# Kernel optimization log

Hardware: AMD Instinct MI355X
Metric: run time of the kernel (lower is better)

The kernel has to match this reference:

```python
import jax, jax.numpy as jnp
import numpy as np

N_ROI = 1024
N_CLASS = 21      # num_classes + 1
APP_DIM = 1024
D_F = 128
N_REL = 16
DIM_K = 64
DIM_G = 64


def loc2bbox(src, loc):
    # src, loc: [M,4] with (y0,x0,y1,x1) / (dy,dx,dh,dw)
    h = src[:, 2] - src[:, 0]
    w = src[:, 3] - src[:, 1]
    cy = src[:, 0] + 0.5 * h
    cx = src[:, 1] + 0.5 * w
    ncy = loc[:, 0] * h + cy
    ncx = loc[:, 1] * w + cx
    nh = jnp.exp(loc[:, 2]) * h
    nw = jnp.exp(loc[:, 3]) * w
    return jnp.stack([ncy - 0.5 * nh, ncx - 0.5 * nw,
                      ncy + 0.5 * nh, ncx + 0.5 * nw], axis=1)


def rank_embedding(n, feat_dim, wave_len=1000.0):
    rank = jnp.arange(n, dtype=jnp.float32)[:, None]
    fr = jnp.arange(feat_dim // 2, dtype=jnp.float32)
    dim_mat = 1.0 / (wave_len ** (fr / (feat_dim / 2.0)))
    mul = rank * dim_mat[None, :]
    return jnp.concatenate([jnp.sin(mul), jnp.cos(mul)], axis=-1)  # [n, feat_dim]


def positional_embedding(f_g, dim_g, wave_len=1000.0):
    # f_g: [N,4]; replicates the repo's PositionalEmbedding exactly
    x_min, y_min, x_max, y_max = jnp.split(f_g, 4, axis=1)  # [N,1] each
    cx = (x_min + x_max) * 0.5
    cy = (y_min + y_max) * 0.5
    w = (x_max - x_min) + 1.0
    h = (y_max - y_min) + 1.0
    dx = jnp.log(jnp.maximum(jnp.abs((cx - cx.T) / w), 1e-3))
    dy = jnp.log(jnp.maximum(jnp.abs((cy - cy.T) / h), 1e-3))
    dw = jnp.log(w / w.T)
    dh = jnp.log(h / h.T)
    pos = jnp.stack([dx, dy, dw, dh], axis=-1)               # [N,N,4]
    fr = jnp.arange(dim_g // 8, dtype=jnp.float32)
    dim_mat = 1.0 / (wave_len ** (fr / (dim_g / 8.0)))       # [dim_g/8]
    mul = (100.0 * pos)[..., None] * dim_mat                 # [N,N,4,dim_g/8]
    mul = mul.reshape(pos.shape[0], pos.shape[1], -1)
    return jnp.concatenate([jnp.sin(mul), jnp.cos(mul)], axis=-1)  # [N,N,dim_g]


def setup_inputs():
    key = jax.random.key(0)
    ks = jax.random.split(key, 16)
    yx = jax.random.uniform(ks[0], (N_ROI, 2), minval=0.0, maxval=500.0)
    hw = jax.random.uniform(ks[1], (N_ROI, 2), minval=16.0, maxval=128.0)
    sample_roi = jnp.concatenate([yx, yx + hw], axis=1)      # valid (y0,x0,y1,x1)
    roi_cls_loc = jax.random.normal(ks[2], (N_ROI, N_CLASS * 4)) * 0.5
    roi_score = jax.random.normal(ks[3], (N_ROI, N_CLASS))
    # force no background argmax -> nonzero() filter keeps all N (static shapes)
    roi_score = roi_score.at[:, 0].add(-10.0)
    appearance_features = jax.random.normal(ks[4], (N_ROI, APP_DIM))
    size = jnp.array([600, 800], dtype=jnp.int32)
    s = 0.02
    rank_w = jax.random.normal(ks[5], (APP_DIM, D_F)) * s
    rank_b = jnp.zeros((D_F,), jnp.float32)
    feat_w = jax.random.normal(ks[6], (APP_DIM, D_F)) * s
    feat_b = jnp.zeros((D_F,), jnp.float32)
    logit_w = jax.random.normal(ks[7], (APP_DIM, 1)) * s
    logit_b = jnp.zeros((1,), jnp.float32)
    wg_w = jax.random.normal(ks[8], (N_REL, DIM_G)) * s
    wg_b = jnp.full((N_REL,), 0.1, jnp.float32)  # keep some geo weights > 0
    wk_w = jax.random.normal(ks[9], (N_REL, D_F, DIM_K)) * s
    wk_b = jnp.zeros((N_REL, DIM_K), jnp.float32)
    wq_w = jax.random.normal(ks[10], (N_REL, D_F, DIM_K)) * s
    wq_b = jnp.zeros((N_REL, DIM_K), jnp.float32)
    wv_w = jax.random.normal(ks[11], (N_REL, D_F, DIM_K)) * s
    wv_b = jnp.zeros((N_REL, DIM_K), jnp.float32)
    return {"sample_roi": sample_roi, "roi_cls_loc": roi_cls_loc,
            "roi_score": roi_score, "appearance_features": appearance_features,
            "size": size,
            "rank_w": rank_w, "rank_b": rank_b, "feat_w": feat_w, "feat_b": feat_b,
            "logit_w": logit_w, "logit_b": logit_b,
            "wg_w": wg_w, "wg_b": wg_b, "wk_w": wk_w, "wk_b": wk_b,
            "wq_w": wq_w, "wq_b": wq_b, "wv_w": wv_w, "wv_b": wv_b}


def reference(sample_roi, roi_cls_loc, roi_score, appearance_features, size,
              rank_w, rank_b, feat_w, feat_b, logit_w, logit_b,
              wg_w, wg_b, wk_w, wk_b, wq_w, wq_b, wv_w, wv_b):
    n = sample_roi.shape[0]
    size_f = size.astype(jnp.float32)
    # loc denormalization (mean = 0)
    std = jnp.tile(jnp.array([0.1, 0.1, 0.2, 0.2], jnp.float32), N_CLASS)
    loc = (roi_cls_loc * std).reshape(-1, 4)                  # [N*21,4]
    roi_rep = jnp.broadcast_to(sample_roi[:, None, :], (n, N_CLASS, 4)).reshape(-1, 4)
    cls_bbox = loc2bbox(roi_rep, loc).reshape(n, N_CLASS, 4)
    # replicates original's clamp on class-strided slices of the [N,21,4] view
    cls_bbox = cls_bbox.at[:, 0::2].set(jnp.clip(cls_bbox[:, 0::2], 0.0, size_f[0]))
    cls_bbox = cls_bbox.at[:, 1::2].set(jnp.clip(cls_bbox[:, 1::2], 0.0, size_f[1]))
    prob_all = jax.nn.softmax(roi_score, axis=1)
    prob = jnp.max(prob_all, axis=-1)
    prob_argmax = jnp.argmax(prob_all, axis=-1)
    cls_bbox = cls_bbox[jnp.arange(n), prob_argmax]           # [N,4]
    # background filter; inputs guarantee all foreground -> static size n
    nz = jnp.nonzero(prob_argmax, size=n, fill_value=0)[0]
    prob_argmax = prob_argmax[nz]
    prob = prob[nz]
    cls_bbox = cls_bbox[nz]
    feats = appearance_features[nz]
    order = jnp.argsort(-prob)                                # descending
    sorted_prob = prob[order]
    sorted_cls_bboxes = cls_bbox[order]
    sorted_labels = prob_argmax[order]
    sorted_features = feats[order]
    nms_rank = rank_embedding(n, APP_DIM) @ rank_w + rank_b   # [N,D_F]
    emb_feat = sorted_features @ feat_w + feat_b + nms_rank   # [N,D_F]
    pos_emb = positional_embedding(sorted_cls_bboxes, DIM_G)  # [N,N,DIM_G]
    # 16 independent RelationUnits, batched as heads h
    w_g = jax.nn.relu(jnp.einsum('mng,hg->hmn', pos_emb, wg_w) + wg_b[:, None, None])
    k = jnp.einsum('nd,hdk->hnk', emb_feat, wk_w) + wk_b[:, None, :]
    q = jnp.einsum('nd,hdk->hnk', emb_feat, wq_w) + wq_b[:, None, :]
    v = jnp.einsum('nd,hdk->hnk', emb_feat, wv_w) + wv_b[:, None, :]
    # scaled_dot[m,n] = k_m . q_n (row m is 'key', softmax over n) per original
    scores = jnp.einsum('hmk,hnk->hmn', k, q) / np.sqrt(DIM_K).astype(np.float32)
    w_mn = jax.nn.softmax(jnp.log(jnp.maximum(w_g, 1e-6)) + scores, axis=-1)
    rel = jnp.einsum('hmn,hnk->hmk', w_mn, v)                 # [H,N,K]
    rel = rel.transpose(1, 0, 2).reshape(n, N_REL * DIM_K) + sorted_features
    s1 = jax.nn.sigmoid(rel @ logit_w + logit_b).reshape(-1)
    nms_scores = s1 * sorted_prob
    return nms_scores, sorted_labels - 1, sorted_cls_bboxes
```

## Files before the change

kernel.cpp:

```cpp
#include <hip/hip_runtime.h>
#include <hip/hip_bf16.h>
#include <math.h>

typedef unsigned long long u64;
typedef unsigned int u32;
typedef __hip_bfloat16 bf16;

#define N 1024
#define NCLS 21
#define APP 1024
#define DF 128
#define NH 16
#define DK 64
#define NS 4

typedef __attribute__((ext_vector_type(8))) short short8v;
typedef __attribute__((ext_vector_type(4))) float float4v;
union U4S8 { uint4 u; short8v s; };

__device__ __forceinline__ float b2f(bf16 x) { return __bfloat162float(x); }
__device__ __forceinline__ ushort f2bu(float x) { bf16 b = __float2bfloat16(x); return *(ushort*)&b; }
__device__ __forceinline__ float bu2f(ushort u) { return __uint_as_float(((uint)u) << 16); }

__global__ void k_prep(const float* __restrict__ roi, const float* __restrict__ cls_loc,
                       const float* __restrict__ score, const int* __restrict__ size,
                       const float* __restrict__ wgw,
                       float* __restrict__ prob, int* __restrict__ label,
                       float* __restrict__ bbox, u64* __restrict__ keys,
                       ushort* __restrict__ wgwb)
{
    int i = blockIdx.x * 256 + threadIdx.x;
    if (i >= N) return;
    wgwb[i] = f2bu(wgw[i]);

    float s[NCLS];
    float mx = -1e30f; int am = 0;
    for (int c = 0; c < NCLS; c++) {
        s[c] = score[i * NCLS + c];
        if (s[c] > mx) { mx = s[c]; am = c; }
    }
    float sum = 0.f;
    for (int c = 0; c < NCLS; c++) sum += expf(s[c] - mx);
    float p = 1.0f / sum;

    float y0 = roi[i*4+0], x0 = roi[i*4+1];
    float y1 = roi[i*4+2], x1 = roi[i*4+3];
    float hh = y1 - y0, ww = x1 - x0;
    float cy = y0 + 0.5f * hh, cx = x0 + 0.5f * ww;
    float l0 = cls_loc[i*84 + am*4 + 0] * 0.1f;
    float l1 = cls_loc[i*84 + am*4 + 1] * 0.1f;
    float l2 = cls_loc[i*84 + am*4 + 2] * 0.2f;
    float l3 = cls_loc[i*84 + am*4 + 3] * 0.2f;
    float ncy = l0 * hh + cy, ncx = l1 * ww + cx;
    float nh = expf(l2) * hh, nw = expf(l3) * ww;
    float b0 = ncy - 0.5f * nh, b1 = ncx - 0.5f * nw;
    float b2v = ncy + 0.5f * nh, b3 = ncx + 0.5f * nw;
    float lim = ((am & 1) == 0) ? (float)size[0] : (float)size[1];
    b0  = fminf(fmaxf(b0, 0.f), lim);
    b1  = fminf(fmaxf(b1, 0.f), lim);
    b2v = fminf(fmaxf(b2v, 0.f), lim);
    b3  = fminf(fmaxf(b3, 0.f), lim);
    prob[i] = p; label[i] = am;
    bbox[i*4+0] = b0; bbox[i*4+1] = b1; bbox[i*4+2] = b2v; bbox[i*4+3] = b3;
    keys[i] = ((u64)(0xFFFFFFFFu - __float_as_uint(p)) << 32) | (u32)i;
}

__global__ void __launch_bounds__(256) k_rank(
        const u64* __restrict__ keys, const float* __restrict__ prob,
        const int* __restrict__ label, const float* __restrict__ bbox,
        int* __restrict__ order, float* __restrict__ sprob,
        float* __restrict__ sbbox, float* __restrict__ sgeo,
        float* __restrict__ out)
{
    __shared__ u64 sk[N];
    int t = threadIdx.x;
    int i = blockIdx.x * 256 + t;
    for (int j = t; j < N; j += 256) sk[j] = keys[j];
    __syncthreads();
    u64 my = sk[i];
    int r = 0;
    for (int j = 0; j < N; j++) r += (sk[j] < my) ? 1 : 0;
    order[r] = i;
    sprob[r] = prob[i];
    float b0 = bbox[i*4+0], b1 = bbox[i*4+1], b2 = bbox[i*4+2], b3 = bbox[i*4+3];
    sbbox[r*4+0] = b0; sbbox[r*4+1] = b1; sbbox[r*4+2] = b2; sbbox[r*4+3] = b3;
    sgeo[r*4+0] = (b0 + b2) * 0.5f;
    sgeo[r*4+1] = (b1 + b3) * 0.5f;
    sgeo[r*4+2] = __logf(b2 - b0 + 1.0f);
    sgeo[r*4+3] = __logf(b3 - b1 + 1.0f);
    out[N + r] = (float)(label[i] - 1);
    out[2*N + r*4 + 0] = b0;
    out[2*N + r*4 + 1] = b1;
    out[2*N + r*4 + 2] = b2;
    out[2*N + r*4 + 3] = b3;
}

__global__ void __launch_bounds__(256) k_geoemb(
        const int* __restrict__ order, const float* __restrict__ app,
        const float* __restrict__ feat_w, const float* __restrict__ rank_w,
        float* __restrict__ part,
        const float* __restrict__ sbbox, const float* __restrict__ sgeo,
        const ushort* __restrict__ wgwb,
        const float* __restrict__ wgb, bf16* __restrict__ lw)
{
    __shared__ __align__(16) char smem[27904];
    int bx = blockIdx.x, t = threadIdx.x;
    int w = t >> 6, l = t & 63, l15 = l & 15, quad = l >> 4;

    if (bx >= 256) {
        uint (*sOut)[260] = (uint(*)[260])smem;
        int m = bx - 256;

        float4 mg = *(const float4*)&sgeo[m*4];
        float4 mb = *(const float4*)&sbbox[m*4];
        float wm = mb.z - mb.x + 1.0f, hm = mb.w - mb.y + 1.0f;

        float sC  = (quad == 0) ? mg.x : (quad == 1) ? mg.y : 0.0f;
        float sM  = ((quad & 1) == 0) ? 1e-3f * wm : 1e-3f * hm;
        float sL  = ((quad & 1) == 0) ? mg.z : mg.w;
        float sSg = (quad < 2) ? 100.0f : -100.0f;

        U4S8 Bg0, Bg1;
        const uint4* wg4 = (const uint4*)wgwb;
        Bg0.u = wg4[l15*8 + quad];
        Bg1.u = wg4[l15*8 + 4 + quad];
        float bias = wgb[l15];

        const float dmt[8] = { 1.0f, 0.42169650342f, 0.177827941f, 0.0749894209f,
                               0.0316227766f, 0.01333521432f, 0.00562341325f, 0.00237137371f };

        uint* lwu = (uint*)lw;
        for (int half = 0; half < 2; half++) {
            #pragma unroll 4
            for (int mt2i = 0; mt2i < 8; mt2i++) {
                int mt2 = half*8 + mt2i;
                int n = mt2*64 + w*16 + l15;
                float valn = sgeo[n*4 + quad];
                float lg = __logf(fmaxf(fabsf(sC - valn), sM));
                float lv = (quad < 2) ? lg : valn;
                float P  = sSg * (lv - sL);

                U4S8 Af0, Af1;
                #pragma unroll
                for (int j = 0; j < 4; j++) {
                    float s0, c0, s1, c1;
                    __sincosf(P * dmt[2*j],     &s0, &c0);
                    __sincosf(P * dmt[2*j + 1], &s1, &c1);
                    ((uint*)&Af0)[j] = (uint)f2bu(s0) | ((uint)f2bu(s1) << 16);
                    ((uint*)&Af1)[j] = (uint)f2bu(c0) | ((uint)f2bu(c1) << 16);
                }

                float4v c = (float4v){0.f, 0.f, 0.f, 0.f};
                c = __builtin_amdgcn_mfma_f32_16x16x32_bf16(Af0.s, Bg0.s, c, 0, 0, 0);
                c = __builtin_amdgcn_mfma_f32_16x16x32_bf16(Af1.s, Bg1.s, c, 0, 0, 0);
                float v0 = __logf(fmaxf(c[0] + bias, 1e-6f));
                float v1 = __logf(fmaxf(c[1] + bias, 1e-6f));
                float v2 = __logf(fmaxf(c[2] + bias, 1e-6f));
                float v3 = __logf(fmaxf(c[3] + bias, 1e-6f));
                int pb = mt2i*32 + w*8 + quad*2;
                sOut[l15][pb]     = (uint)f2bu(v0) | ((uint)f2bu(v1) << 16);
                sOut[l15][pb + 1] = (uint)f2bu(v2) | ((uint)f2bu(v3) << 16);
            }
            __syncthreads();
            #pragma unroll
            for (int it = 0; it < 4; it++) {
                int idx = t + it * 256;
                int hh = idx >> 6, col4 = idx & 63;
                uint4 val = *(const uint4*)&sOut[hh][col4*4];
                *(uint4*)&lwu[((size_t)hh << 19) + ((size_t)m << 9) + half*256 + col4*4] = val;
            }
            __syncthreads();
        }
    } else {
        ushort (*sA)[72] = (ushort(*)[72])smem;
        ushort (*sW)[72] = (ushort(*)[72])(smem + 9216);
        int* sOrd = (int*)(smem + 27648);
        int idx0 = bx;
        int rt = idx0 & 15, dg = (idx0 >> 4) & 7, ph = idx0 >> 7;
        int r0 = rt * 64;
        if (t < 64) sOrd[t] = order[r0 + t];
        __syncthreads();

        const float* Wsrc = ph ? rank_w : feat_w;
        float4v acc[8];
        #pragma unroll
        for (int nb = 0; nb < 8; nb++) acc[nb] = (float4v){0.f, 0.f, 0.f, 0.f};

        for (int dc = dg * 2; dc < dg * 2 + 2; dc++) {
            int d0 = dc * 64;
            #pragma unroll
            for (int it = 0; it < 32; it++) {
                int idx = t + it * 256;
                int d = idx >> 7, c = idx & 127;
                sW[c][d] = f2bu(Wsrc[(size_t)(d0 + d) * 128 + c]);
            }
            if (ph == 0) {
                #pragma unroll
                for (int it = 0; it < 16; it++) {
                    int idx = t + it * 256;
                    int r = idx >> 6, d = idx & 63;
                    sA[r][d] = f2bu(app[(size_t)sOrd[r] * 1024 + d0 + d]);
                }
            } else {
                #pragma unroll
                for (int it = 0; it < 16; it++) {
                    int idx = t + it * 256;
                    int r = idx >> 6, d = idx & 63;
                    int dgl = d0 + d;
                    float irow = (float)(r0 + r);
                    float val;
                    if (dgl < 512) val = __sinf(irow * exp2f(-(float)dgl * 0.019464422f));
                    else           val = __cosf(irow * exp2f(-(float)(dgl - 512) * 0.019464422f));
                    sA[r][d] = f2bu(val);
                }
            }
            __syncthreads();
            U4S8 Af0, Af1;
            Af0.u = *(uint4*)&sA[w*16 + l15][quad*8];
            Af1.u = *(uint4*)&sA[w*16 + l15][32 + quad*8];
            #pragma unroll
            for (int nb = 0; nb < 8; nb++) {
                U4S8 Bf0, Bf1;
                Bf0.u = *(uint4*)&sW[nb*16 + l15][quad*8];
                Bf1.u = *(uint4*)&sW[nb*16 + l15][32 + quad*8];
                acc[nb] = __builtin_amdgcn_mfma_f32_16x16x32_bf16(Af0.s, Bf0.s, acc[nb], 0, 0, 0);
                acc[nb] = __builtin_amdgcn_mfma_f32_16x16x32_bf16(Af1.s, Bf1.s, acc[nb], 0, 0, 0);
            }
            __syncthreads();
        }
        #pragma unroll
        for (int reg = 0; reg < 4; reg++) {
            int row = r0 + w*16 + quad*4 + reg;
            #pragma unroll
            for (int nb = 0; nb < 8; nb++)
                part[(((size_t)ph * 8 + dg) * 1024 + row) * 128 + nb*16 + l15] = acc[nb][reg];
        }
    }
}

__global__ void k_embsum(const float* __restrict__ part,
                         const float* __restrict__ feat_b, const float* __restrict__ rank_b,
                         bf16* __restrict__ embb)
{
    int gid = blockIdx.x * 256 + threadIdx.x;
    int c = gid & 127;
    float acc = feat_b[c] + rank_b[c];
    #pragma unroll
    for (int p8 = 0; p8 < 16; p8++) acc += part[(size_t)p8 * 131072 + gid];
    embb[gid] = __float2bfloat16(acc);
}

__global__ void __launch_bounds__(256) k_qkv2(
        const bf16* __restrict__ embb,
        const float* __restrict__ wq, const float* __restrict__ bq,
        const float* __restrict__ wk, const float* __restrict__ bk,
        const float* __restrict__ wv, const float* __restrict__ bv,
        bf16* __restrict__ q, bf16* __restrict__ k, bf16* __restrict__ v)
{
    __shared__ ushort sWt[64][136];
    int t = threadIdx.x;
    int rt = blockIdx.x, h = blockIdx.y, mat = blockIdx.z;
    const float* W  = (mat == 0) ? wq : (mat == 1) ? wk : wv;
    const float* Bb = (mat == 0) ? bq : (mat == 1) ? bk : bv;
    bf16* Out       = (mat == 0) ? q  : (mat == 1) ? k  : v;

    #pragma unroll
    for (int i = 0; i < 32; i++) {
        int idx = t + i * 256;
        int d = idx >> 6, kk = idx & 63;
        sWt[kk][d] = f2bu(W[((size_t)h * 128 + d) * 64 + kk]);
    }
    int w = t >> 6, l = t & 63, l15 = l & 15, quad = l >> 4;
    float biasv[4];
    #pragma unroll
    for (int nb = 0; nb < 4; nb++) biasv[nb] = Bb[h * 64 + nb*16 + l15];
    __syncthreads();

    U4S8 Bf[4][4];
    #pragma unroll
    for (int nb = 0; nb < 4; nb++)
        #pragma unroll
        for (int kc = 0; kc < 4; kc++)
            Bf[nb][kc].u = *(uint4*)&sWt[nb*16 + l15][kc*32 + quad*8];

    const uint4* A4 = (const uint4*)embb;
    int r0 = rt * 128 + w * 32;
    ushort* outu = (ushort*)Out;
    for (int mb = 0; mb < 2; mb++) {
        int arow = r0 + mb*16 + l15;
        U4S8 Af[4];
        #pragma unroll
        for (int kc = 0; kc < 4; kc++) Af[kc].u = A4[(size_t)arow * 16 + kc*4 + quad];
        float4v acc[4];
        #pragma unroll
        for (int nb = 0; nb < 4; nb++) acc[nb] = (float4v){0.f, 0.f, 0.f, 0.f};
        #pragma unroll
        for (int kc = 0; kc < 4; kc++)
            #pragma unroll
            for (int nb = 0; nb < 4; nb++)
                acc[nb] = __builtin_amdgcn_mfma_f32_16x16x32_bf16(Af[kc].s, Bf[nb][kc].s, acc[nb], 0, 0, 0);
        #pragma unroll
        for (int reg = 0; reg < 4; reg++) {
            int orow = r0 + mb*16 + quad*4 + reg;
            #pragma unroll
            for (int nb = 0; nb < 4; nb++)
                outu[((size_t)h * N + orow) * 64 + nb*16 + l15] = f2bu(acc[nb][reg] + biasv[nb]);
        }
    }
}

__global__ void __launch_bounds__(256) k_attn4(
        const bf16* __restrict__ q, const bf16* __restrict__ kmat,
        const bf16* __restrict__ v, const bf16* __restrict__ lw,
        bf16* __restrict__ opartb, float* __restrict__ mpart, float* __restrict__ zpart)
{
    __shared__ uint sQu[64][36];
    __shared__ uint sVtu[64][36];
    __shared__ uint slwu[64][36];
    __shared__ uint sPu[4][16][36];

    int t = threadIdx.x;
    int mt = blockIdx.x, h = blockIdx.y, ns = blockIdx.z;
    int m0 = mt * 64;
    int w = t >> 6, l = t & 63, l15 = l & 15, quad = l >> 4;

    U4S8 kf0, kf1;
    {
        const uint4* k4 = (const uint4*)kmat;
        size_t krow = ((size_t)h * N + m0 + w*16 + l15) * 8;
        kf0.u = k4[krow + quad];
        kf1.u = k4[krow + 4 + quad];
    }

    float4v O[4];
    float M[4], Z[4];
    #pragma unroll
    for (int i = 0; i < 4; i++) {
        O[i] = (float4v){0.f, 0.f, 0.f, 0.f};
        M[i] = -1e30f; Z[i] = 0.f;
    }

    const uint* qsrc = (const uint*)q;
    const uint* vsrc = (const uint*)v;
    const uint* lwsrc = (const uint*)lw;

    for (int tile = ns * (16/NS); tile < (ns + 1) * (16/NS); tile++) {
        int n0 = tile * 64;
        #pragma unroll
        for (int i = 0; i < 8; i++) {
            int idx = t + i * 256;
            int nj = idx >> 5, kp = idx & 31;
            sQu[nj][kp] = qsrc[((size_t)h * N + n0 + nj) * 32 + kp];
        }
        #pragma unroll
        for (int i = 0; i < 4; i++) {
            int idx = t + i * 256;
            int a = idx & 31, nh2 = idx >> 5;
            uint g0 = vsrc[((size_t)h * N + n0 + 2*nh2) * 32 + a];
            uint g1 = vsrc[((size_t)h * N + n0 + 2*nh2 + 1) * 32 + a];
            sVtu[2*a][nh2]     = (g0 & 0xFFFFu) | (g1 << 16);
            sVtu[2*a + 1][nh2] = (g0 >> 16) | (g1 & 0xFFFF0000u);
        }
        #pragma unroll
        for (int i = 0; i < 8; i++) {
            int idx = t + i * 256;
            int mi = idx >> 5, np = idx & 31;
            slwu[mi][np] = lwsrc[((size_t)h << 19) + ((size_t)(m0 + mi) << 9) + (n0 >> 1) + np];
        }
        __syncthreads();

        float4v S[4];
        #pragma unroll
        for (int nb = 0; nb < 4; nb++) {
            U4S8 bq0, bq1;
            bq0.u = *(uint4*)&sQu[nb*16 + l15][quad*4];
            bq1.u = *(uint4*)&sQu[nb*16 + l15][16 + quad*4];
            float4v zz = (float4v){0.f, 0.f, 0.f, 0.f};
            float4v p0 = __builtin_amdgcn_mfma_f32_16x16x32_bf16(kf0.s, bq0.s, zz, 0, 0, 0);
            S[nb] = __builtin_amdgcn_mfma_f32_16x16x32_bf16(kf1.s, bq1.s, p0, 0, 0, 0);
        }
        ushort* pRow[4];
        #pragma unroll
        for (int r = 0; r < 4; r++) pRow[r] = (ushort*)&sPu[w][quad*4 + r][0];
        #pragma unroll
        for (int r = 0; r < 4; r++) {
            int mi = w*16 + quad*4 + r;
            float sv[4];
            #pragma unroll
            for (int nb = 0; nb < 4; nb++) {
                int col = nb*16 + l15;
                uint lu = slwu[mi][col >> 1];
                float lv = (col & 1) ? __uint_as_float(lu & 0xFFFF0000u)
                                     : __uint_as_float(lu << 16);
                sv[nb] = S[nb][r] * 0.125f + lv;
            }
            float rm = fmaxf(fmaxf(sv[0], sv[1]), fmaxf(sv[2], sv[3]));
            #pragma unroll
            for (int off = 1; off < 16; off <<= 1)
                rm = fmaxf(rm, __shfl_xor(rm, off, 64));
            float newM = fmaxf(M[r], rm);
            float pr[4], rs = 0.f;
            #pragma unroll
            for (int nb = 0; nb < 4; nb++) {
                pr[nb] = __expf(sv[nb] - newM);
                rs += pr[nb];
            }
            #pragma unroll
            for (int off = 1; off < 16; off <<= 1)
                rs += __shfl_xor(rs, off, 64);
            float sc = __expf(M[r] - newM);
            M[r] = newM;
            Z[r] = Z[r] * sc + rs;
            #pragma unroll
            for (int kvb = 0; kvb < 4; kvb++) O[kvb][r] *= sc;
            #pragma unroll
            for (int nb = 0; nb < 4; nb++)
                pRow[r][nb*16 + l15] = f2bu(pr[nb]);
        }
        {
            U4S8 ap0, ap1;
            ap0.u = *(uint4*)&sPu[w][l15][quad*4];
            ap1.u = *(uint4*)&sPu[w][l15][16 + quad*4];
            #pragma unroll
            for (int kvb = 0; kvb < 4; kvb++) {
                U4S8 bv0, bv1;
                bv0.u = *(uint4*)&sVtu[kvb*16 + l15][quad*4];
                bv1.u = *(uint4*)&sVtu[kvb*16 + l15][16 + quad*4];
                O[kvb] = __builtin_amdgcn_mfma_f32_16x16x32_bf16(ap0.s, bv0.s, O[kvb], 0, 0, 0);
                O[kvb] = __builtin_amdgcn_mfma_f32_16x16x32_bf16(ap1.s, bv1.s, O[kvb], 0, 0, 0);
            }
        }
        __syncthreads();
    }

    ushort* ob = (ushort*)opartb;
    #pragma unroll
    for (int r = 0; r < 4; r++) {
        int m = m0 + w*16 + quad*4 + r;
        size_t row = ((size_t)ns * NH + h) * N + m;
        #pragma unroll
        for (int kvb = 0; kvb < 4; kvb++)
            ob[row * 64 + kvb*16 + l15] = f2bu(O[kvb][r]);
        if (l15 == 0) { mpart[row] = M[r]; zpart[row] = Z[r]; }
    }
}

__global__ void __launch_bounds__(128) k_final2(
        const bf16* __restrict__ opartb, const float* __restrict__ mpart,
        const float* __restrict__ zpart, const int* __restrict__ order,
        const float* __restrict__ app, const float* __restrict__ lw,
        const float* __restrict__ lb, const float* __restrict__ sprob,
        float* __restrict__ out)
{
    __shared__ float sWgt[NH][NS];
    __shared__ float sInvZ[NH];
    __shared__ float red[2];
    int m = blockIdx.x, t = threadIdx.x;
    if (t < NH) {
        int h = t;
        float Ms[NS], Mg = -1e30f;
        #pragma unroll
        for (int ns = 0; ns < NS; ns++) {
            Ms[ns] = mpart[(size_t)ns * 16384 + h * 1024 + m];
            Mg = fmaxf(Mg, Ms[ns]);
        }
        float Zt = 0.f;
        #pragma unroll
        for (int ns = 0; ns < NS; ns++) {
            float wgt = __expf(Ms[ns] - Mg);
            sWgt[h][ns] = wgt;
            Zt += zpart[(size_t)ns * 16384 + h * 1024 + m] * wgt;
        }
        sInvZ[h] = 1.0f / Zt;
    }
    __syncthreads();
    int o = order[m];
    const ushort* ob = (const ushort*)opartb;
    float s = 0.f;
    for (int j = t; j < APP; j += 128) {
        int hh = j >> 6, kk = j & 63;
        size_t base = ((size_t)hh * 1024 + m) * 64 + kk;
        float val = 0.f;
        #pragma unroll
        for (int ns = 0; ns < NS; ns++)
            val += bu2f(ob[(size_t)ns * 1048576 + base]) * sWgt[hh][ns];
        float rv = val * sInvZ[hh] + app[o * APP + j];
        s += rv * lw[j];
    }
    #pragma unroll
    for (int off = 32; off > 0; off >>= 1) s += __shfl_down(s, off, 64);
    if ((t & 63) == 0) red[t >> 6] = s;
    __syncthreads();
    if (t == 0) {
        float tot = red[0] + red[1] + lb[0];
        float s1 = 1.0f / (1.0f + expf(-tot));
        out[m] = s1 * sprob[m];
    }
}

extern "C" void kernel_launch(void* const* d_in, const int* in_sizes, int n_in,
                              void* d_out, int out_size, void* d_ws, size_t ws_size,
                              hipStream_t stream)
{
    const float* roi      = (const float*)d_in[0];
    const float* cls_loc  = (const float*)d_in[1];
    const float* score    = (const float*)d_in[2];
    const float* app      = (const float*)d_in[3];
    const int*   size     = (const int*)d_in[4];
    const float* rank_w   = (const float*)d_in[5];
    const float* rank_b   = (const float*)d_in[6];
    const float* feat_w   = (const float*)d_in[7];
    const float* feat_b   = (const float*)d_in[8];
    const float* logit_w  = (const float*)d_in[9];
    const float* logit_b  = (const float*)d_in[10];
    const float* wg_w     = (const float*)d_in[11];
    const float* wg_b     = (const float*)d_in[12];
    const float* wk_w     = (const float*)d_in[13];
    const float* wk_b     = (const float*)d_in[14];
    const float* wq_w     = (const float*)d_in[15];
    const float* wq_b     = (const float*)d_in[16];
    const float* wv_w     = (const float*)d_in[17];
    const float* wv_b     = (const float*)d_in[18];
    float* out = (float*)d_out;

    char* ws = (char*)d_ws;
    float* prob  = (float*)(ws + 0);
    int*   label = (int*)  (ws + 4096);
    float* bbox  = (float*)(ws + 8192);
    u64*   keys  = (u64*)  (ws + 24576);
    int*   order = (int*)  (ws + 32768);
    float* sprob = (float*)(ws + 36864);
    float* sbbox = (float*)(ws + 40960);
    bf16*  embb  = (bf16*) (ws + 57344);
    ushort* wgwb = (ushort*)(ws + 1048576);
    float* sgeo  = (float*)(ws + 1052672);
    bf16*  q     = (bf16*) (ws + 8970240);
    bf16*  k     = (bf16*) (ws + 11067392);
    bf16*  v     = (bf16*) (ws + 13164544);
    bf16*  lwbuf = (bf16*) (ws + 17358848);
    float* part  = (float*)(ws + 50913280);
    bf16*  opartb= (bf16*) (ws + 67690496);
    float* mpart = (float*)(ws + 84467712);
    float* zpart = (float*)(ws + 84729856);

    k_prep<<<4, 256, 0, stream>>>(roi, cls_loc, score, size, wg_w, prob, label, bbox, keys, wgwb);
    k_rank<<<4, 256, 0, stream>>>(keys, prob, label, bbox, order, sprob, sbbox, sgeo, out);
    k_geoemb<<<1280, 256, 0, stream>>>(order, app, feat_w, rank_w, part,
                                       sbbox, sgeo, wgwb, wg_b, lwbuf);
    k_embsum<<<512, 256, 0, stream>>>(part, feat_b, rank_b, embb);
    k_qkv2<<<dim3(8, 16, 3), 256, 0, stream>>>(embb, wq_w, wq_b, wk_w, wk_b, wv_w, wv_b, q, k, v);
    k_attn4<<<dim3(16, 16, NS), 256, 0, stream>>>(q, k, v, lwbuf, opartb, mpart, zpart);
    k_final2<<<1024, 128, 0, stream>>>(opartb, mpart, zpart, order, app, logit_w, logit_b, sprob, out);
}
```

Baseline: 177.2 us.

## Pre-transpose QKV weights to bf16 once and read Q fragments directly from global

The embedding-sum kernel gets extra blocks that convert and transpose the Q/K/V weights into a bf16 [mat][h][k][d] buffer in workspace. The QKV projection kernel then loads its MFMA B fragments straight from that buffer, with no per-block fp32 transposition through shared memory and no barrier. Separately, the attention kernel stops staging Q tiles in shared memory and loads the Q fragments for each tile directly from global memory. This trades LDS traffic and a sync for more uncoalesced 16-byte global loads, which rely on cache hits.

```diff
diff --git a/kernel.cpp b/kernel.cpp
--- a/kernel.cpp
+++ b/kernel.cpp
@@ -240,48 +240,54 @@
 
 __global__ void k_embsum(const float* __restrict__ part,
                          const float* __restrict__ feat_b, const float* __restrict__ rank_b,
-                         bf16* __restrict__ embb)
-{
-    int gid = blockIdx.x * 256 + threadIdx.x;
-    int c = gid & 127;
-    float acc = feat_b[c] + rank_b[c];
-    #pragma unroll
-    for (int p8 = 0; p8 < 16; p8++) acc += part[(size_t)p8 * 131072 + gid];
-    embb[gid] = __float2bfloat16(acc);
+                         bf16* __restrict__ embb,
+                         const float* __restrict__ wq, const float* __restrict__ wk,
+                         const float* __restrict__ wv, ushort* __restrict__ wqkvt)
+{
+    int b = blockIdx.x, t = threadIdx.x;
+    if (b < 512) {
+        int gid = b * 256 + t;
+        int c = gid & 127;
+        float acc = feat_b[c] + rank_b[c];
+        #pragma unroll
+        for (int p8 = 0; p8 < 16; p8++) acc += part[(size_t)p8 * 131072 + gid];
+        embb[gid] = __float2bfloat16(acc);
+    } else {
+        int lin = (b - 512) * 256 + t;
+        int mat = lin >> 17;
+        int rem = lin & 131071;
+        int h   = rem >> 13;
+        int rem2 = rem & 8191;
+        int kk  = rem2 >> 7;
+        int d   = rem2 & 127;
+        const float* W = (mat == 0) ? wq : (mat == 1) ? wk : wv;
+        wqkvt[lin] = f2bu(W[(((size_t)h * 128 + d) << 6) + kk]);
+    }
 }
 
 __global__ void __launch_bounds__(256) k_qkv2(
-        const bf16* __restrict__ embb,
-        const float* __restrict__ wq, const float* __restrict__ bq,
-        const float* __restrict__ wk, const float* __restrict__ bk,
-        const float* __restrict__ wv, const float* __restrict__ bv,
+        const bf16* __restrict__ embb, const ushort* __restrict__ wqkvt,
+        const float* __restrict__ bq, const float* __restrict__ bk,
+        const float* __restrict__ bv,
         bf16* __restrict__ q, bf16* __restrict__ k, bf16* __restrict__ v)
 {
-    __shared__ ushort sWt[64][136];
     int t = threadIdx.x;
     int rt = blockIdx.x, h = blockIdx.y, mat = blockIdx.z;
-    const float* W  = (mat == 0) ? wq : (mat == 1) ? wk : wv;
     const float* Bb = (mat == 0) ? bq : (mat == 1) ? bk : bv;
     bf16* Out       = (mat == 0) ? q  : (mat == 1) ? k  : v;
-
+    int w = t >> 6, l = t & 63, l15 = l & 15, quad = l >> 4;
+
+    const uint4* Wt4 = (const uint4*)(wqkvt + ((size_t)(mat * 16 + h) << 13));
+    U4S8 Bf[4][4];
     #pragma unroll
-    for (int i = 0; i < 32; i++) {
-        int idx = t + i * 256;
-        int d = idx >> 6, kk = idx & 63;
-        sWt[kk][d] = f2bu(W[((size_t)h * 128 + d) * 64 + kk]);
-    }
-    int w = t >> 6, l = t & 63, l15 = l & 15, quad = l >> 4;
+    for (int nb = 0; nb < 4; nb++)
+        #pragma unroll
+        for (int kc = 0; kc < 4; kc++)
+            Bf[nb][kc].u = Wt4[(nb*16 + l15) * 16 + kc*4 + quad];
+
     float biasv[4];
     #pragma unroll
     for (int nb = 0; nb < 4; nb++) biasv[nb] = Bb[h * 64 + nb*16 + l15];
-    __syncthreads();
-
-    U4S8 Bf[4][4];
-    #pragma unroll
-    for (int nb = 0; nb < 4; nb++)
-        #pragma unroll
-        for (int kc = 0; kc < 4; kc++)
-            Bf[nb][kc].u = *(uint4*)&sWt[nb*16 + l15][kc*32 + quad*8];
 
     const uint4* A4 = (const uint4*)embb;
     int r0 = rt * 128 + w * 32;
@@ -314,7 +320,6 @@
         const bf16* __restrict__ v, const bf16* __restrict__ lw,
         bf16* __restrict__ opartb, float* __restrict__ mpart, float* __restrict__ zpart)
 {
-    __shared__ uint sQu[64][36];
     __shared__ uint sVtu[64][36];
     __shared__ uint slwu[64][36];
     __shared__ uint sPu[4][16][36];
@@ -325,8 +330,9 @@
     int w = t >> 6, l = t & 63, l15 = l & 15, quad = l >> 4;
 
     U4S8 kf0, kf1;
+    const uint4* k4 = (const uint4*)kmat;
+    const uint4* q4 = (const uint4*)q;
     {
-        const uint4* k4 = (const uint4*)kmat;
         size_t krow = ((size_t)h * N + m0 + w*16 + l15) * 8;
         kf0.u = k4[krow + quad];
         kf1.u = k4[krow + 4 + quad];
@@ -340,18 +346,11 @@
         M[i] = -1e30f; Z[i] = 0.f;
     }
 
-    const uint* qsrc = (const uint*)q;
     const uint* vsrc = (const uint*)v;
     const uint* lwsrc = (const uint*)lw;
 
     for (int tile = ns * (16/NS); tile < (ns + 1) * (16/NS); tile++) {
         int n0 = tile * 64;
-        #pragma unroll
-        for (int i = 0; i < 8; i++) {
-            int idx = t + i * 256;
-            int nj = idx >> 5, kp = idx & 31;
-            sQu[nj][kp] = qsrc[((size_t)h * N + n0 + nj) * 32 + kp];
-        }
         #pragma unroll
         for (int i = 0; i < 4; i++) {
             int idx = t + i * 256;
@@ -373,8 +372,9 @@
         #pragma unroll
         for (int nb = 0; nb < 4; nb++) {
             U4S8 bq0, bq1;
-            bq0.u = *(uint4*)&sQu[nb*16 + l15][quad*4];
-            bq1.u = *(uint4*)&sQu[nb*16 + l15][16 + quad*4];
+            size_t qrow = ((size_t)h * N + n0 + nb*16 + l15) * 8;
+            bq0.u = q4[qrow + quad];
+            bq1.u = q4[qrow + 4 + quad];
             float4v zz = (float4v){0.f, 0.f, 0.f, 0.f};
             float4v p0 = __builtin_amdgcn_mfma_f32_16x16x32_bf16(kf0.s, bq0.s, zz, 0, 0, 0);
             S[nb] = __builtin_amdgcn_mfma_f32_16x16x32_bf16(kf1.s, bq1.s, p0, 0, 0, 0);
@@ -534,6 +534,7 @@
     bf16*  embb  = (bf16*) (ws + 57344);
     ushort* wgwb = (ushort*)(ws + 1048576);
     float* sgeo  = (float*)(ws + 1052672);
+    ushort* wqkvt= (ushort*)(ws + 2097152);
     bf16*  q     = (bf16*) (ws + 8970240);
     bf16*  k     = (bf16*) (ws + 11067392);
     bf16*  v     = (bf16*) (ws + 13164544);
@@ -547,8 +548,8 @@
     k_rank<<<4, 256, 0, stream>>>(keys, prob, label, bbox, order, sprob, sbbox, sgeo, out);
     k_geoemb<<<1280, 256, 0, stream>>>(order, app, feat_w, rank_w, part,
                                        sbbox, sgeo, wgwb, wg_b, lwbuf);
-    k_embsum<<<512, 256, 0, stream>>>(part, feat_b, rank_b, embb);
-    k_qkv2<<<dim3(8, 16, 3), 256, 0, stream>>>(embb, wq_w, wq_b, wk_w, wk_b, wv_w, wv_b, q, k, v);
+    k_embsum<<<2048, 256, 0, stream>>>(part, feat_b, rank_b, embb, wq_w, wk_w, wv_w, wqkvt);
+    k_qkv2<<<dim3(8, 16, 3), 256, 0, stream>>>(embb, wqkvt, wq_b, wk_b, wv_b, q, k, v);
     k_attn4<<<dim3(16, 16, NS), 256, 0, stream>>>(q, k, v, lwbuf, opartb, mpart, zpart);
     k_final2<<<1024, 128, 0, stream>>>(opartb, mpart, zpart, order, app, logit_w, logit_b, sprob, out);
 }
```

Result: slower. 185.3 us (+4.6%).
